# Optimization experiments

Measured on AMD Instinct MI355X. Metric: run time of the kernel, lower is better.

Reference implementation:

```python
import jax, jax.numpy as jnp
import numpy as np

# Hyperparameters (from init_kwargs)
B, N, K = 4, 16384, 16          # batch, points, kNN neighbors
C_IN, C_OUT = 64, 128           # in_planes, out_planes
KSIZE, DIL, STRIDE = 9, 1, 1    # WeightedConv1D kernel
PAD = DIL * (KSIZE // 2)        # padding = dilation*(k//2)
SIGMA = 0.02
NEG_SLOPE = 0.2                 # leakyrelu default in DeepGCN BasicConv
EPS = 1e-5                      # BatchNorm eps


def setup_inputs() -> dict:
    key = jax.random.key(0)
    ks = jax.random.split(key, 6)
    x = jax.random.normal(ks[0], (B, C_IN, N), jnp.float32)
    coords = jax.random.uniform(ks[1], (B, 3, N), jnp.float32)
    edge_index = jax.random.randint(ks[2], (2, B, N, K), 0, N)
    # EdgeConv MLP: Conv2d(2*C_IN, C_IN, 1, bias=False) -> BN -> LeakyReLU
    w_edge = jax.random.normal(ks[3], (C_IN, 2 * C_IN), jnp.float32) * (1.0 / np.sqrt(2 * C_IN))
    bn_gamma = jnp.ones((C_IN,), jnp.float32)
    bn_beta = jnp.zeros((C_IN,), jnp.float32)
    # WeightedConv1D learned kernel [C_out, C_in, k] + bias
    w_conv = jax.random.normal(ks[4], (C_OUT, C_IN, KSIZE), jnp.float32) * (1.0 / np.sqrt(C_IN * KSIZE))
    b_conv = jnp.zeros((C_OUT,), jnp.float32)
    return dict(x=x, coords=coords, edge_index=edge_index, w_edge=w_edge,
                bn_gamma=bn_gamma, bn_beta=bn_beta, w_conv=w_conv, b_conv=b_conv)


def _edge_conv(x, edge_index, w_edge, gamma, beta):
    # x: [B, C, N]; edge_index: [2, B, N, K]
    x_t = jnp.transpose(x, (0, 2, 1))                        # [B, N, C]
    gather = jax.vmap(lambda xt, idx: xt[idx])               # ([N,C],[N,K]) -> [N,K,C]
    x_j = gather(x_t, edge_index[0])                         # neighbor feats [B,N,K,C]
    x_i = gather(x_t, edge_index[1])                         # center feats   [B,N,K,C]
    feat = jnp.concatenate([x_i, x_j - x_i], axis=-1)        # [B,N,K,2C]
    h = jnp.einsum('bnkc,oc->bnko', feat, w_edge)            # 1x1 conv, bias=False
    # BatchNorm2d (training-mode batch stats over B,N,K per channel)
    mean = jnp.mean(h, axis=(0, 1, 2))
    var = jnp.var(h, axis=(0, 1, 2))
    h = (h - mean) * jax.lax.rsqrt(var + EPS) * gamma + beta
    h = jnp.where(h >= 0, h, NEG_SLOPE * h)                  # leaky_relu(0.2)
    return jnp.transpose(jnp.max(h, axis=2), (0, 2, 1))      # max over K -> [B,C,N]


def _weighted_conv(x, coords, w_conv, b_conv):
    # x: [B, C, N]; coords: [B, 3, N]
    xp = jnp.pad(x, ((0, 0), (0, 0), (PAD, PAD)))
    cp = jnp.pad(coords, ((0, 0), (0, 0), (PAD, PAD)))
    # unfold into k shifted views (k is small and static)
    x_win = jnp.stack([xp[:, :, j * DIL: j * DIL + N] for j in range(KSIZE)], axis=2)  # [B,C,k,N]
    c_win = jnp.stack([cp[:, :, j * DIL: j * DIL + N] for j in range(KSIZE)], axis=2)  # [B,3,k,N]
    d2 = jnp.sum((c_win - coords[:, :, None, :]) ** 2, axis=1)                          # [B,k,N]
    w = jnp.exp(-d2 / (SIGMA ** 2))                           # Gaussian coord weights
    out = jnp.einsum('bcjn,ocj->bon', x_win * w[:, None], w_conv)
    return out + b_conv[None, :, None]                        # [B, C_out, N]


def reference(x, coords, edge_index, w_edge, bn_gamma, bn_beta, w_conv, b_conv):
    h = _edge_conv(x, edge_index, w_edge, bn_gamma, bn_beta)
    return _weighted_conv(h, coords, w_conv, b_conv)
```

## Files before the change

kernel.cpp:

```cpp
#include <hip/hip_runtime.h>
#include <hip/hip_bf16.h>

#define B_ 4
#define N_ 16384
#define K_ 16
#define NEG 0.2f
#define EPSBN 1e-5f
#define INV_SIG2 2500.0f

typedef unsigned short u16;
typedef unsigned int   u32;
typedef __attribute__((ext_vector_type(8))) short short8;
typedef __attribute__((ext_vector_type(4))) float f32x4;

__device__ __forceinline__ float bf2f(u16 h){
  return __uint_as_float(((u32)h) << 16);
}
__device__ __forceinline__ u16 f2bf(float f){
  u32 x = __float_as_uint(f);
  x += 0x7fffu + ((x >> 16) & 1u);
  return (u16)(x >> 16);
}


__global__ void k0_wprep(const float* __restrict__ wconv, u16* __restrict__ wbf,
                         const float* __restrict__ we, u16* __restrict__ weA,
                         float* __restrict__ stats){
  const int idx = blockIdx.x * 256 + threadIdx.x;
  if (idx < 128) stats[idx] = 0.f;
  if (idx < 9*128*64){
    const int j = idx >> 13;
    const int rem = idx & 8191;
    const int o = rem >> 6, c = rem & 63;
    wbf[idx] = f2bf(wconv[(o*64 + c)*9 + j]);
  } else if (idx < 9*128*64 + 128*64){
    const int t = idx - 9*128*64;
    const int o = t >> 6, c = t & 63;
    float w;
    if (o < 64) w = we[o*128 + c] - we[o*128 + 64 + c];
    else        w = we[(o-64)*128 + 64 + c];
    weA[t] = f2bf(w);
  }
}

__global__ __launch_bounds__(256) void k1_uv(const float* __restrict__ x,
                                             const u16* __restrict__ weA,
                                             u16* __restrict__ uo,
                                             u16* __restrict__ vo){
  const int n0 = blockIdx.x * 64;
  const int b  = blockIdx.y;
  const int tid = threadIdx.x;
  const int w = tid >> 6, lane = tid & 63;
  const int r15 = lane & 15, kg = lane >> 4;

  __shared__ u16 tl[128*72];

  short8 a[2][2];
  #pragma unroll
  for (int of = 0; of < 2; ++of)
    #pragma unroll
    for (int kh = 0; kh < 2; ++kh)
      a[of][kh] = *(const short8*)&weA[(w*32 + of*16 + r15)*64 + kg*8 + kh*32];

  const float* xb = x + (size_t)b*64*N_ + n0 + r15;
  f32x4 acc[2][4];
  const f32x4 zero = {0.f, 0.f, 0.f, 0.f};

  #pragma unroll
  for (int nf = 0; nf < 4; ++nf){
    short8 bq[2];
    #pragma unroll
    for (int kh = 0; kh < 2; ++kh){
      float f[8];
      #pragma unroll
      for (int e = 0; e < 8; ++e)
        f[e] = xb[(size_t)(kg*8 + kh*32 + e)*N_ + nf*16];
      union { short8 s; u32 u[4]; } bb;
      #pragma unroll
      for (int e2 = 0; e2 < 4; ++e2)
        bb.u[e2] = (u32)f2bf(f[e2*2]) | ((u32)f2bf(f[e2*2+1]) << 16);
      bq[kh] = bb.s;
    }
    #pragma unroll
    for (int of = 0; of < 2; ++of){
      f32x4 p = __builtin_amdgcn_mfma_f32_16x16x32_bf16(a[of][0], bq[0], zero, 0, 0, 0);
      acc[of][nf] = __builtin_amdgcn_mfma_f32_16x16x32_bf16(a[of][1], bq[1], p, 0, 0, 0);
    }
  }

  #pragma unroll
  for (int of = 0; of < 2; ++of)
    #pragma unroll
    for (int rr = 0; rr < 4; ++rr){
      const int o = w*32 + of*16 + kg*4 + rr;
      #pragma unroll
      for (int nf = 0; nf < 4; ++nf)
        tl[o*72 + nf*16 + r15] = f2bf(acc[of][nf][rr]);
    }
  __syncthreads();

  const int arr = tid >> 7, half = (tid >> 6) & 1, n = tid & 63;
  const int ro = arr*64 + half*32;
  u32 pk[16];
  #pragma unroll
  for (int cc = 0; cc < 16; ++cc){
    const u16 lo = tl[(ro + cc*2    )*72 + n];
    const u16 hi = tl[(ro + cc*2 + 1)*72 + n];
    pk[cc] = (u32)lo | ((u32)hi << 16);
  }
  u16* dst = (arr ? vo : uo) + ((size_t)(half*B_ + b)*N_ + n0 + n)*32;
  *(uint4*)(dst +  0) = make_uint4(pk[0],  pk[1],  pk[2],  pk[3]);
  *(uint4*)(dst +  8) = make_uint4(pk[4],  pk[5],  pk[6],  pk[7]);
  *(uint4*)(dst + 16) = make_uint4(pk[8],  pk[9],  pk[10], pk[11]);
  *(uint4*)(dst + 24) = make_uint4(pk[12], pk[13], pk[14], pk[15]);
}

__global__ __launch_bounds__(256) void k2_gather(const u16* __restrict__ uo,
                                                 const u16* __restrict__ vo,
                                                 const int* __restrict__ eidx,
                                                 u16* __restrict__ wmaxo,
                                                 u16* __restrict__ wmino,
                                                 float* __restrict__ stats){
  const int bid = blockIdx.x;
  const int p8  = bid & 7;
  const int b   = p8 >> 1;
  const int h   = p8 & 1;
  const int n0  = (bid >> 3) * 32;
  const int tid = threadIdx.x;
  const int wid = tid >> 6, lane = tid & 63;
  const int kk = lane >> 4, cg = lane & 15;
  const int nb = n0 + wid*8;
  const size_t pbase = ((size_t)(h*B_ + b))*N_*32;
  const u16* ub = uo + pbase;
  const u16* vb = vo + pbase;

  __shared__ int eL[4][2][128];
  __shared__ float redS[4][32], redQ[4][32];

  const int* e0 = eidx + (b*N_ + nb)*K_;
  const int* e1 = eidx + B_*N_*K_ + (b*N_ + nb)*K_;
  if (lane < 32) *(int4*)&eL[wid][0][lane*4]      = *(const int4*)(e0 + lane*4);
  else           *(int4*)&eL[wid][1][(lane-32)*4] = *(const int4*)(e1 + (lane-32)*4);
  __syncthreads();

  float s0=0.f, s1=0.f, q0=0.f, q1=0.f;

  for (int p = 0; p < 8; ++p){
    int ji[4], ii[4];
    #pragma unroll
    for (int s = 0; s < 4; ++s){
      ji[s] = eL[wid][0][p*16 + s*4 + kk];
      ii[s] = eL[wid][1][p*16 + s*4 + kk];
    }
    u32 ua[4], va[4];
    #pragma unroll
    for (int s = 0; s < 4; ++s){
      ua[s] = __builtin_nontemporal_load((const u32*)&ub[(size_t)ii[s]*32 + cg*2]);
      va[s] = __builtin_nontemporal_load((const u32*)&vb[(size_t)ji[s]*32 + cg*2]);
    }
    float hL[4], hH[4];
    #pragma unroll
    for (int s = 0; s < 4; ++s){
      hL[s] = __uint_as_float(ua[s] << 16)         + __uint_as_float(va[s] << 16);
      hH[s] = __uint_as_float(ua[s] & 0xffff0000u) + __uint_as_float(va[s] & 0xffff0000u);
    }
    float mx0 = fmaxf(fmaxf(hL[0],hL[1]), fmaxf(hL[2],hL[3]));
    float mn0 = fminf(fminf(hL[0],hL[1]), fminf(hL[2],hL[3]));
    float mx1 = fmaxf(fmaxf(hH[0],hH[1]), fmaxf(hH[2],hH[3]));
    float mn1 = fminf(fminf(hH[0],hH[1]), fminf(hH[2],hH[3]));
    s0 += (hL[0]+hL[1]) + (hL[2]+hL[3]);
    s1 += (hH[0]+hH[1]) + (hH[2]+hH[3]);
    q0 = fmaf(hL[0],hL[0], fmaf(hL[1],hL[1], fmaf(hL[2],hL[2], fmaf(hL[3],hL[3], q0))));
    q1 = fmaf(hH[0],hH[0], fmaf(hH[1],hH[1], fmaf(hH[2],hH[2], fmaf(hH[3],hH[3], q1))));
    mx0 = fmaxf(mx0, __shfl_xor(mx0, 16)); mx0 = fmaxf(mx0, __shfl_xor(mx0, 32));
    mx1 = fmaxf(mx1, __shfl_xor(mx1, 16)); mx1 = fmaxf(mx1, __shfl_xor(mx1, 32));
    mn0 = fminf(mn0, __shfl_xor(mn0, 16)); mn0 = fminf(mn0, __shfl_xor(mn0, 32));
    mn1 = fminf(mn1, __shfl_xor(mn1, 16)); mn1 = fminf(mn1, __shfl_xor(mn1, 32));
    const int n = nb + p;
    if (lane < 16){
      const u32 pm = (u32)f2bf(mx0) | ((u32)f2bf(mx1) << 16);
      const u32 pn = (u32)f2bf(mn0) | ((u32)f2bf(mn1) << 16);
      *(u32*)&wmaxo[pbase + (size_t)n*32 + cg*2] = pm;
      *(u32*)&wmino[pbase + (size_t)n*32 + cg*2] = pn;
    }
  }

  s0 += __shfl_xor(s0,16); s0 += __shfl_xor(s0,32);
  s1 += __shfl_xor(s1,16); s1 += __shfl_xor(s1,32);
  q0 += __shfl_xor(q0,16); q0 += __shfl_xor(q0,32);
  q1 += __shfl_xor(q1,16); q1 += __shfl_xor(q1,32);
  if (lane < 16){
    redS[wid][cg*2]   = s0;  redS[wid][cg*2+1] = s1;
    redQ[wid][cg*2]   = q0;  redQ[wid][cg*2+1] = q1;
  }
  __syncthreads();
  if (tid < 32){
    atomicAdd(&stats[h*32 + tid], redS[0][tid]+redS[1][tid]+redS[2][tid]+redS[3][tid]);
  } else if (tid < 64){
    const int c = tid - 32;
    atomicAdd(&stats[64 + h*32 + c], redQ[0][c]+redQ[1][c]+redQ[2][c]+redQ[3][c]);
  }
}

__global__ __launch_bounds__(256) void k4_mfma(const u16* __restrict__ wmaxo,
                                               const u16* __restrict__ wmino,
                                               const float* __restrict__ stats,
                                               const float* __restrict__ gamma,
                                               const float* __restrict__ beta,
                                               const float* __restrict__ coords,
                                               const u16* __restrict__ wbf,
                                               const float* __restrict__ bconv,
                                               float* __restrict__ out){
  const int n0 = blockIdx.x * 64;
  const int b  = blockIdx.y;
  const int tid = threadIdx.x;
  const int w = tid >> 6, lane = tid & 63;
  const int r15 = lane & 15, kg = lane >> 4;

  __shared__ u16 hl[72*72];
  __shared__ float wgt[9*64];
  __shared__ float sctl[128];

  if (tid < 64){
    const float inv = 1.0f / (float)(B_*N_*K_);
    const float mean = stats[tid] * inv;
    const float var  = stats[64+tid] * inv - mean*mean;
    const float s = gamma[tid] * rsqrtf(var + EPSBN);
    sctl[tid] = s;
    sctl[64+tid] = beta[tid] - mean*s;
  }
  __syncthreads();

  {
    const int c = tid & 63;
    const float s = sctl[c], t = sctl[64+c];
    const u16* src = ((s >= 0.f) ? wmaxo : wmino)
                   + ((size_t)((c >> 5)*B_ + b))*N_*32 + (c & 31);
    #pragma unroll
    for (int it = 0; it < 18; ++it){
      const int ml = (tid >> 6) + it*4;
      const int m = n0 - 4 + ml;
      float hv = 0.f;
      if (m >= 0 && m < N_){
        hv = fmaf(s, bf2f(src[(size_t)m*32]), t);
        hv = (hv >= 0.f) ? hv : NEG*hv;
      }
      hl[ml*72 + c] = f2bf(hv);
    }
  }
  for (int idx = tid; idx < 576; idx += 256){
    const int j = idx >> 6, n = idx & 63;
    const int mc = n0 + n, mt = mc + j - 4;
    float wv = 0.f;
    if (mt >= 0 && mt < N_){
      float d2 = 0.f;
      #pragma unroll
      for (int d = 0; d < 3; ++d){
        const float dd = coords[(b*3+d)*N_ + mt] - coords[(b*3+d)*N_ + mc];
        d2 = fmaf(dd, dd, d2);
      }
      wv = __expf(-INV_SIG2 * d2);
    }
    wgt[idx] = wv;
  }
  __syncthreads();

  const u16* abase = wbf + ((w*32 + r15)*64 + kg*8);
  const u16* hbase = &hl[r15*72 + kg*8];
  f32x4 acc[2][4] = {};
  const f32x4 zero = {0.f, 0.f, 0.f, 0.f};

  for (int j = 0; j < 9; ++j){
    float wj[4];
    #pragma unroll
    for (int nf = 0; nf < 4; ++nf) wj[nf] = wgt[j*64 + nf*16 + r15];
    short8 bfr[4][2];
    #pragma unroll
    for (int nf = 0; nf < 4; ++nf){
      bfr[nf][0] = *(const short8*)&hbase[(nf*16 + j)*72];
      bfr[nf][1] = *(const short8*)&hbase[(nf*16 + j)*72 + 32];
    }
    #pragma unroll
    for (int of = 0; of < 2; ++of){
      const short8 a0 = *(const short8*)&abase[j*8192 + of*1024];
      const short8 a1 = *(const short8*)&abase[j*8192 + of*1024 + 32];
      #pragma unroll
      for (int nf = 0; nf < 4; ++nf){
        f32x4 p = __builtin_amdgcn_mfma_f32_16x16x32_bf16(a0, bfr[nf][0], zero, 0, 0, 0);
        p = __builtin_amdgcn_mfma_f32_16x16x32_bf16(a1, bfr[nf][1], p, 0, 0, 0);
        #pragma unroll
        for (int r = 0; r < 4; ++r)
          acc[of][nf][r] = fmaf(wj[nf], p[r], acc[of][nf][r]);
      }
    }
  }

  #pragma unroll
  for (int of = 0; of < 2; ++of){
    #pragma unroll
    for (int r = 0; r < 4; ++r){
      const int o = w*32 + of*16 + kg*4 + r;
      const float bs = bconv[o];
      float* dst = &out[(size_t)(b*128 + o)*N_ + n0 + r15];
      #pragma unroll
      for (int nf = 0; nf < 4; ++nf)
        dst[nf*16] = acc[of][nf][r] + bs;
    }
  }
}

extern "C" void kernel_launch(void* const* d_in, const int* in_sizes, int n_in,
                              void* d_out, int out_size, void* d_ws, size_t ws_size,
                              hipStream_t stream){
  const float* x      = (const float*)d_in[0];
  const float* coords = (const float*)d_in[1];
  const int*   eidx   = (const int*)  d_in[2];
  const float* we     = (const float*)d_in[3];
  const float* gamma  = (const float*)d_in[4];
  const float* beta   = (const float*)d_in[5];
  const float* wconv  = (const float*)d_in[6];
  const float* bconv  = (const float*)d_in[7];
  float* out = (float*)d_out;
  char* ws = (char*)d_ws;
  u16* u     = (u16*)(ws);
  u16* v     = (u16*)(ws + 8388608);
  u16* wmax_ = (u16*)(ws + 16777216);
  u16* wmin_ = (u16*)(ws + 25165824);
  float* stats = (float*)(ws + 33554432);
  u16* wbf     = (u16*)(ws + 33555456);
  u16* weA     = (u16*)(ws + 33555456 + 147456);

  k0_wprep<<<320, 256, 0, stream>>>(wconv, wbf, we, weA, stats);
  k1_uv<<<dim3(N_/64, B_), 256, 0, stream>>>(x, weA, u, v);
  k2_gather<<<4096, 256, 0, stream>>>(u, v, eidx, wmax_, wmin_, stats);
  k4_mfma<<<dim3(N_/64, B_), 256, 0, stream>>>(wmax_, wmin_, stats, gamma, beta,
                                               coords, wbf, bconv, out);
}
```

Before: 130.0 us.

## Interleave u/v channel halves per point so gather fetches all 64 channels

The intermediate u/v arrays change from two planes of 32 channels to one row of 64 channels per point. The gather kernel now covers both channel halves in one block, reading 8 bytes per lane instead of 4 and launching half as many blocks. Each random neighbor index therefore costs one 128-byte row fetch rather than two separate 64-byte fetches, and the edge indices are loaded once instead of twice. In exchange each lane holds more registers, the nontemporal load hint is dropped, and the max/min output layout stays split by half so the final conv kernel is unchanged.

```diff
diff --git a/kernel.cpp b/kernel.cpp
--- a/kernel.cpp
+++ b/kernel.cpp
@@ -99,8 +99,8 @@
     }
   __syncthreads();
 
-  const int arr = tid >> 7, half = (tid >> 6) & 1, n = tid & 63;
-  const int ro = arr*64 + half*32;
+  const int arr = tid >> 7, nh = (tid >> 6) & 1, n = tid & 63;
+  const int ro = arr*64 + nh*32;
   u32 pk[16];
   #pragma unroll
   for (int cc = 0; cc < 16; ++cc){
@@ -108,7 +108,7 @@
     const u16 hi = tl[(ro + cc*2 + 1)*72 + n];
     pk[cc] = (u32)lo | ((u32)hi << 16);
   }
-  u16* dst = (arr ? vo : uo) + ((size_t)(half*B_ + b)*N_ + n0 + n)*32;
+  u16* dst = (arr ? vo : uo) + ((size_t)(b*N_ + n0 + n))*64 + nh*32;
   *(uint4*)(dst +  0) = make_uint4(pk[0],  pk[1],  pk[2],  pk[3]);
   *(uint4*)(dst +  8) = make_uint4(pk[4],  pk[5],  pk[6],  pk[7]);
   *(uint4*)(dst + 16) = make_uint4(pk[8],  pk[9],  pk[10], pk[11]);
@@ -122,20 +122,18 @@
                                                  u16* __restrict__ wmino,
                                                  float* __restrict__ stats){
   const int bid = blockIdx.x;
-  const int p8  = bid & 7;
-  const int b   = p8 >> 1;
-  const int h   = p8 & 1;
-  const int n0  = (bid >> 3) * 32;
+  const int xcd = bid & 7;
+  const int b   = xcd >> 1;
+  const int n0  = ((bid >> 3) + (xcd & 1)*256) * 32;
   const int tid = threadIdx.x;
   const int wid = tid >> 6, lane = tid & 63;
   const int kk = lane >> 4, cg = lane & 15;
   const int nb = n0 + wid*8;
-  const size_t pbase = ((size_t)(h*B_ + b))*N_*32;
-  const u16* ub = uo + pbase;
-  const u16* vb = vo + pbase;
+  const u16* ub = uo + (size_t)b*N_*64;
+  const u16* vb = vo + (size_t)b*N_*64;
 
   __shared__ int eL[4][2][128];
-  __shared__ float redS[4][32], redQ[4][32];
+  __shared__ float redS[4][64], redQ[4][64];
 
   const int* e0 = eidx + (b*N_ + nb)*K_;
   const int* e1 = eidx + B_*N_*K_ + (b*N_ + nb)*K_;
@@ -143,7 +141,7 @@
   else           *(int4*)&eL[wid][1][(lane-32)*4] = *(const int4*)(e1 + (lane-32)*4);
   __syncthreads();
 
-  float s0=0.f, s1=0.f, q0=0.f, q1=0.f;
+  float sm[4] = {0.f,0.f,0.f,0.f}, sq[4] = {0.f,0.f,0.f,0.f};
 
   for (int p = 0; p < 8; ++p){
     int ji[4], ii[4];
@@ -152,53 +150,65 @@
       ji[s] = eL[wid][0][p*16 + s*4 + kk];
       ii[s] = eL[wid][1][p*16 + s*4 + kk];
     }
-    u32 ua[4], va[4];
+    uint2 ua[4], va[4];
     #pragma unroll
     for (int s = 0; s < 4; ++s){
-      ua[s] = __builtin_nontemporal_load((const u32*)&ub[(size_t)ii[s]*32 + cg*2]);
-      va[s] = __builtin_nontemporal_load((const u32*)&vb[(size_t)ji[s]*32 + cg*2]);
-    }
-    float hL[4], hH[4];
+      ua[s] = *(const uint2*)&ub[(size_t)ii[s]*64 + cg*4];
+      va[s] = *(const uint2*)&vb[(size_t)ji[s]*64 + cg*4];
+    }
+    float h[4][4];
     #pragma unroll
     for (int s = 0; s < 4; ++s){
-      hL[s] = __uint_as_float(ua[s] << 16)         + __uint_as_float(va[s] << 16);
-      hH[s] = __uint_as_float(ua[s] & 0xffff0000u) + __uint_as_float(va[s] & 0xffff0000u);
-    }
-    float mx0 = fmaxf(fmaxf(hL[0],hL[1]), fmaxf(hL[2],hL[3]));
-    float mn0 = fminf(fminf(hL[0],hL[1]), fminf(hL[2],hL[3]));
-    float mx1 = fmaxf(fmaxf(hH[0],hH[1]), fmaxf(hH[2],hH[3]));
-    float mn1 = fminf(fminf(hH[0],hH[1]), fminf(hH[2],hH[3]));
-    s0 += (hL[0]+hL[1]) + (hL[2]+hL[3]);
-    s1 += (hH[0]+hH[1]) + (hH[2]+hH[3]);
-    q0 = fmaf(hL[0],hL[0], fmaf(hL[1],hL[1], fmaf(hL[2],hL[2], fmaf(hL[3],hL[3], q0))));
-    q1 = fmaf(hH[0],hH[0], fmaf(hH[1],hH[1], fmaf(hH[2],hH[2], fmaf(hH[3],hH[3], q1))));
-    mx0 = fmaxf(mx0, __shfl_xor(mx0, 16)); mx0 = fmaxf(mx0, __shfl_xor(mx0, 32));
-    mx1 = fmaxf(mx1, __shfl_xor(mx1, 16)); mx1 = fmaxf(mx1, __shfl_xor(mx1, 32));
-    mn0 = fminf(mn0, __shfl_xor(mn0, 16)); mn0 = fminf(mn0, __shfl_xor(mn0, 32));
-    mn1 = fminf(mn1, __shfl_xor(mn1, 16)); mn1 = fminf(mn1, __shfl_xor(mn1, 32));
+      h[s][0] = __uint_as_float(ua[s].x << 16)         + __uint_as_float(va[s].x << 16);
+      h[s][1] = __uint_as_float(ua[s].x & 0xffff0000u) + __uint_as_float(va[s].x & 0xffff0000u);
+      h[s][2] = __uint_as_float(ua[s].y << 16)         + __uint_as_float(va[s].y << 16);
+      h[s][3] = __uint_as_float(ua[s].y & 0xffff0000u) + __uint_as_float(va[s].y & 0xffff0000u);
+    }
+    float mx[4], mn[4];
+    #pragma unroll
+    for (int c = 0; c < 4; ++c){
+      mx[c] = fmaxf(fmaxf(h[0][c],h[1][c]), fmaxf(h[2][c],h[3][c]));
+      mn[c] = fminf(fminf(h[0][c],h[1][c]), fminf(h[2][c],h[3][c]));
+      sm[c] += (h[0][c]+h[1][c]) + (h[2][c]+h[3][c]);
+      sq[c] = fmaf(h[0][c],h[0][c], fmaf(h[1][c],h[1][c],
+              fmaf(h[2][c],h[2][c], fmaf(h[3][c],h[3][c], sq[c]))));
+      mx[c] = fmaxf(mx[c], __shfl_xor(mx[c],16)); mx[c] = fmaxf(mx[c], __shfl_xor(mx[c],32));
+      mn[c] = fminf(mn[c], __shfl_xor(mn[c],16)); mn[c] = fminf(mn[c], __shfl_xor(mn[c],32));
+    }
     const int n = nb + p;
-    if (lane < 16){
-      const u32 pm = (u32)f2bf(mx0) | ((u32)f2bf(mx1) << 16);
-      const u32 pn = (u32)f2bf(mn0) | ((u32)f2bf(mn1) << 16);
-      *(u32*)&wmaxo[pbase + (size_t)n*32 + cg*2] = pm;
-      *(u32*)&wmino[pbase + (size_t)n*32 + cg*2] = pn;
-    }
-  }
-
-  s0 += __shfl_xor(s0,16); s0 += __shfl_xor(s0,32);
-  s1 += __shfl_xor(s1,16); s1 += __shfl_xor(s1,32);
-  q0 += __shfl_xor(q0,16); q0 += __shfl_xor(q0,32);
-  q1 += __shfl_xor(q1,16); q1 += __shfl_xor(q1,32);
-  if (lane < 16){
-    redS[wid][cg*2]   = s0;  redS[wid][cg*2+1] = s1;
-    redQ[wid][cg*2]   = q0;  redQ[wid][cg*2+1] = q1;
-  }
-  __syncthreads();
-  if (tid < 32){
-    atomicAdd(&stats[h*32 + tid], redS[0][tid]+redS[1][tid]+redS[2][tid]+redS[3][tid]);
-  } else if (tid < 64){
-    const int c = tid - 32;
-    atomicAdd(&stats[64 + h*32 + c], redQ[0][c]+redQ[1][c]+redQ[2][c]+redQ[3][c]);
+    if (kk == 0){
+      const int c0 = cg*4;
+      const int hh = c0 >> 5;
+      u16* wm = wmaxo + ((size_t)(hh*B_ + b)*N_ + n)*32 + (c0 & 31);
+      u16* wn = wmino + ((size_t)(hh*B_ + b)*N_ + n)*32 + (c0 & 31);
+      uint2 pm, pn;
+      pm.x = (u32)f2bf(mx[0]) | ((u32)f2bf(mx[1]) << 16);
+      pm.y = (u32)f2bf(mx[2]) | ((u32)f2bf(mx[3]) << 16);
+      pn.x = (u32)f2bf(mn[0]) | ((u32)f2bf(mn[1]) << 16);
+      pn.y = (u32)f2bf(mn[2]) | ((u32)f2bf(mn[3]) << 16);
+      *(uint2*)wm = pm;
+      *(uint2*)wn = pn;
+    }
+  }
+
+  #pragma unroll
+  for (int c = 0; c < 4; ++c){
+    sm[c] += __shfl_xor(sm[c],16); sm[c] += __shfl_xor(sm[c],32);
+    sq[c] += __shfl_xor(sq[c],16); sq[c] += __shfl_xor(sq[c],32);
+  }
+  if (kk == 0){
+    #pragma unroll
+    for (int c = 0; c < 4; ++c){
+      redS[wid][cg*4 + c] = sm[c];
+      redQ[wid][cg*4 + c] = sq[c];
+    }
+  }
+  __syncthreads();
+  if (tid < 64){
+    atomicAdd(&stats[tid], redS[0][tid]+redS[1][tid]+redS[2][tid]+redS[3][tid]);
+  } else if (tid < 128){
+    const int c = tid - 64;
+    atomicAdd(&stats[64 + c], redQ[0][c]+redQ[1][c]+redQ[2][c]+redQ[3][c]);
   }
 }
 
@@ -332,7 +342,7 @@
 
   k0_wprep<<<320, 256, 0, stream>>>(wconv, wbf, we, weA, stats);
   k1_uv<<<dim3(N_/64, B_), 256, 0, stream>>>(x, weA, u, v);
-  k2_gather<<<4096, 256, 0, stream>>>(u, v, eidx, wmax_, wmin_, stats);
+  k2_gather<<<2048, 256, 0, stream>>>(u, v, eidx, wmax_, wmin_, stats);
   k4_mfma<<<dim3(N_/64, B_), 256, 0, stream>>>(wmax_, wmin_, stats, gamma, beta,
                                                coords, wbf, bconv, out);
 }
```

Measured after the change: 130.3 us. About the same (+0.3%).
